# Optimization experiments

Measured on AMD Instinct MI355X. Metric: run time of the kernel, lower is better.

The kernel has to match this reference:

```python
import jax, jax.numpy as jnp
import numpy as np

TOPK = 9
N_CLASSES = 80
EPS = 1e-9


def bbox_iou(a, b):
    # a [N,4], b [M,4] xyxy -> [N,M]
    lt = jnp.maximum(a[:, None, :2], b[None, :, :2])
    rb = jnp.minimum(a[:, None, 2:], b[None, :, 2:])
    wh = jnp.clip(rb - lt, 0.0)
    inter = wh[..., 0] * wh[..., 1]
    area_a = (a[:, 2] - a[:, 0]) * (a[:, 3] - a[:, 1])
    area_b = (b[:, 2] - b[:, 0]) * (b[:, 3] - b[:, 1])
    return inter / (area_a[:, None] + area_b[None, :] - inter + EPS)


def atss_forward(anchor_bboxes, n_level_bboxes, gt_labels, gt_bboxes, mask_gt, pred_bboxes):
    na = anchor_bboxes.shape[0]
    bs, nmax = gt_bboxes.shape[:2]
    dt = gt_bboxes.dtype
    gt_flat = gt_bboxes.reshape(-1, 4)                       # [bs*nmax, 4]
    overlaps = bbox_iou(gt_flat, anchor_bboxes).reshape(bs, nmax, na)
    gt_c = (gt_flat[:, :2] + gt_flat[:, 2:]) * 0.5           # [bs*nmax, 2]
    an_c = (anchor_bboxes[:, :2] + anchor_bboxes[:, 2:]) * 0.5  # [na, 2]
    distances = jnp.sqrt(((gt_c[:, None, :] - an_c[None, :, :]) ** 2).sum(-1)).reshape(bs, nmax, na)

    # per-level topk candidate selection (levels are static python ints)
    mask_gt_b = mask_gt > 0                                  # [bs, nmax, 1]
    rows = jnp.arange(bs * nmax)[:, None]
    is_in_topk_list, topk_idx_list = [], []
    start = 0
    for nL in n_level_bboxes:
        k = min(TOPK, nL)
        d = distances[..., start:start + nL]
        _, idxs = jax.lax.top_k(-d, k)                       # closest-k -> [bs,nmax,k]
        topk_idx_list.append(idxs + start)
        idx_m = jnp.where(mask_gt_b, idxs, 0).reshape(bs * nmax, k)
        counts = jnp.zeros((bs * nmax, nL), dt).at[rows, idx_m].add(1.0)
        counts = counts.reshape(bs, nmax, nL)
        is_in_topk_list.append(jnp.where(counts > 1, jnp.zeros((), dt), counts))
        start += nL
    is_in_topk = jnp.concatenate(is_in_topk_list, -1)        # [bs,nmax,na]
    topk_idxs = jnp.concatenate(topk_idx_list, -1)           # [bs,nmax,sum_k]

    # adaptive threshold = mean + std of candidate IoUs (unbiased std, as torch)
    cand_ov = jnp.where(is_in_topk > 0, overlaps, 0.0)
    gathered = jnp.take_along_axis(cand_ov.reshape(bs * nmax, na),
                                   topk_idxs.reshape(bs * nmax, -1), axis=1)
    gathered = gathered.reshape(bs, nmax, -1)
    thr = gathered.mean(-1, keepdims=True) + jnp.std(gathered, axis=-1, ddof=1, keepdims=True)
    is_pos = jnp.where(cand_ov > thr, is_in_topk, 0.0)

    # anchor center strictly inside GT box
    lt = an_c[None, :, :] - gt_flat[:, None, :2]
    rb = gt_flat[:, None, 2:] - an_c[None, :, :]
    in_gt = (jnp.concatenate([lt, rb], -1).min(-1) > EPS).astype(dt).reshape(bs, nmax, na)

    mask_pos = is_pos * in_gt * mask_gt                      # mask_gt broadcasts [bs,nmax,1]

    # collision fix: anchors assigned to multiple GTs keep highest-IoU GT
    mps = mask_pos.sum(-2)                                   # [bs, na]
    multi = (mps[:, None, :] > 1)                            # [bs,1,na] broadcast
    is_max = jax.nn.one_hot(overlaps.argmax(1), nmax, dtype=dt).transpose(0, 2, 1)
    mask_pos = jnp.where(multi, is_max, mask_pos)
    mps = mask_pos.sum(-2)
    assigned_gt_idx = mask_pos.argmax(-2)                    # [bs, na]

    # final gathers
    flat_idx = assigned_gt_idx + jnp.arange(bs)[:, None] * nmax
    labels = gt_labels.reshape(-1)[flat_idx]                 # [bs, na]
    boxes = gt_bboxes.reshape(-1, 4)[flat_idx]               # [bs, na, 4]
    labels = jnp.where(mps > 0, labels, N_CLASSES)
    scores = jax.nn.one_hot(labels, N_CLASSES + 1, dtype=dt)[..., :N_CLASSES]

    # rescale scores by IoU(gt, pred) on positive anchors
    pious = jax.vmap(bbox_iou)(gt_bboxes, pred_bboxes) * mask_pos  # [bs,nmax,na]
    scores = scores * pious.max(-2)[..., None]
    return labels, boxes, scores, (mps > 0)


def setup_inputs():
    key = jax.random.key(0)
    ks = jax.random.split(key, 4)
    bs, nmax, img = 32, 100, 640
    strides = [8, 16, 32]
    anchors, nlb = [], []
    for s in strides:
        n = img // s
        xy = (np.stack(np.meshgrid(np.arange(n), np.arange(n), indexing='ij'), -1)
              .reshape(-1, 2).astype(np.float32) + 0.5) * s
        half = 2.5 * s
        anchors.append(np.concatenate([xy - half, xy + half], -1))
        nlb.append(n * n)
    anchor_bboxes = jnp.asarray(np.concatenate(anchors, 0), jnp.float32)  # [8400,4]
    na = anchor_bboxes.shape[0]

    def rand_boxes(k, shape):
        k1, k2 = jax.random.split(k)
        xy = jax.random.uniform(k1, shape + (2,), jnp.float32) * 520.0
        wh = jax.random.uniform(k2, shape + (2,), jnp.float32) * 112.0 + 8.0
        return jnp.concatenate([xy, xy + wh], -1)

    gt_bboxes = rand_boxes(ks[0], (bs, nmax))
    pred_bboxes = rand_boxes(ks[1], (bs, na))
    gt_labels = jax.random.randint(ks[2], (bs, nmax, 1), 0, N_CLASSES)
    mask_gt = (jax.random.uniform(ks[3], (bs, nmax, 1)) < 0.8).astype(jnp.float32)
    return {"anchor_bboxes": anchor_bboxes, "n_level_bboxes": nlb,
            "gt_labels": gt_labels, "gt_bboxes": gt_bboxes,
            "mask_gt": mask_gt, "pred_bboxes": pred_bboxes}


def reference(anchor_bboxes, n_level_bboxes, gt_labels, gt_bboxes, mask_gt, pred_bboxes):
    return atss_forward(anchor_bboxes, n_level_bboxes, gt_labels, gt_bboxes, mask_gt, pred_bboxes)
```

## Files before the change

### kernel.cpp

```cpp
#include <hip/hip_runtime.h>
#include <cstdint>
#include <cstddef>

#define BS   32
#define NMAX 100
#define NA   8400
#define NTOP 9
#define NLEV 3
#define NCLS 80

#define LAB_OFF 0
#define BOX_OFF (BS * NA)
#define SC_OFF  (BS * NA * 5)
#define FG_OFF  (BS * NA * 5 + BS * NA * NCLS)

__device__ __forceinline__ float iou_ab(float ax1, float ay1, float ax2, float ay2,
                                        float bx1, float by1, float bx2, float by2) {
    float ltx = fmaxf(ax1, bx1), lty = fmaxf(ay1, by1);
    float rbx = fminf(ax2, bx2), rby = fminf(ay2, by2);
    float w = fmaxf(__fsub_rn(rbx, ltx), 0.0f);
    float h = fmaxf(__fsub_rn(rby, lty), 0.0f);
    float inter = __fmul_rn(w, h);
    float aa = __fmul_rn(__fsub_rn(ax2, ax1), __fsub_rn(ay2, ay1));
    float ab = __fmul_rn(__fsub_rn(bx2, bx1), __fsub_rn(by2, by1));
    float den = __fadd_rn(__fadd_rn(__fadd_rn(aa, ab), -inter), 1e-9f);
    return __fdiv_rn(inter, den);
}

__global__ __launch_bounds__(256) void zero_ws(uint4* __restrict__ p, int n4) {
    const int i = blockIdx.x * 256 + threadIdx.x;
    if (i < n4) p[i] = make_uint4(0u, 0u, 0u, 0u);
}

__global__ __launch_bounds__(256) void atss_phase1(
    const float* __restrict__ anchors,
    const float* __restrict__ gt_bboxes,
    const float* __restrict__ mask_gt,
    unsigned* __restrict__ packed)
{
    const int wid  = (blockIdx.x << 2) + (threadIdx.x >> 6);
    const int lane = threadIdx.x & 63;
    if (wid >= BS * NMAX) return;
    if (mask_gt[wid] <= 0.0f) return;
    const int b = wid / NMAX;
    const int g = wid - b * NMAX;

    const float4 gtb = reinterpret_cast<const float4*>(gt_bboxes)[wid];
    const float gx1 = gtb.x, gy1 = gtb.y, gx2 = gtb.z, gy2 = gtb.w;
    const float gcx = __fmul_rn(__fadd_rn(gx1, gx2), 0.5f);
    const float gcy = __fmul_rn(__fadd_rn(gy1, gy2), 0.5f);

    const int   lev_start[NLEV] = {0, 6400, 8000};
    const int   lev_n[NLEV]     = {80, 40, 20};
    const float lev_s[NLEV]     = {8.f, 16.f, 32.f};

    int my_sel = 0;

    for (int L = 0; L < NLEV; ++L) {
        const int   n     = lev_n[L];
        const float s     = lev_s[L];
        const int   start = lev_start[L];

        const int ixn = (int)floorf(gcx / s - 0.5f + 0.5f);
        const int iyn = (int)floorf(gcy / s - 0.5f + 0.5f);
        const int wx = min(max(ixn - 3, 0), n - 7);
        const int wy = min(max(iyn - 3, 0), n - 7);

        unsigned long long key = ~0ull;
        int aidx = 0;
        if (lane < 49) {
            const int cix = wx + lane / 7;
            const int ciy = wy + lane % 7;
            aidx = start + cix * n + ciy;
            const float4 ab = reinterpret_cast<const float4*>(anchors)[aidx];
            const float acx = __fmul_rn(__fadd_rn(ab.x, ab.z), 0.5f);
            const float acy = __fmul_rn(__fadd_rn(ab.y, ab.w), 0.5f);
            const float dx = __fsub_rn(gcx, acx);
            const float dy = __fsub_rn(gcy, acy);
            const float d = sqrtf(__fadd_rn(__fmul_rn(dx, dx), __fmul_rn(dy, dy)));
            key = ((unsigned long long)__float_as_uint(d) << 32) | (unsigned)aidx;
        }

        int rank = 0;
#pragma unroll
        for (int j = 0; j < 49; ++j) {
            const unsigned long long kj = (unsigned long long)__shfl((long long)key, j);
            rank += (kj < key) ? 1 : 0;
        }

        const int dst = (rank < NTOP) ? (L * NTOP + rank) : 63;
        const int got = __builtin_amdgcn_ds_permute(dst << 2, aidx);
        if (lane >= L * NTOP && lane < L * NTOP + NTOP) my_sel = got;
    }

    float ov = 0.0f, acx = 0.0f, acy = 0.0f;
    if (lane < NLEV * NTOP) {
        const float4 ab = reinterpret_cast<const float4*>(anchors)[my_sel];
        ov  = iou_ab(gx1, gy1, gx2, gy2, ab.x, ab.y, ab.z, ab.w);
        acx = __fmul_rn(__fadd_rn(ab.x, ab.z), 0.5f);
        acy = __fmul_rn(__fadd_rn(ab.y, ab.w), 0.5f);
    }

    float sum = 0.0f;
#pragma unroll
    for (int j = 0; j < NLEV * NTOP; ++j) sum = __fadd_rn(sum, __shfl(ov, j));
    const float mean = __fdiv_rn(sum, 27.0f);
    float v = 0.0f;
#pragma unroll
    for (int j = 0; j < NLEV * NTOP; ++j) {
        const float dlt = __fsub_rn(__shfl(ov, j), mean);
        v = __fadd_rn(v, __fmul_rn(dlt, dlt));
    }
    const float thr = __fadd_rn(mean, sqrtf(__fdiv_rn(v, 26.0f)));

    if (lane < NLEV * NTOP && ov > thr) {
        const float m2 = fminf(fminf(__fsub_rn(acx, gx1), __fsub_rn(acy, gy1)),
                               fminf(__fsub_rn(gx2, acx), __fsub_rn(gy2, acy)));
        if (m2 > 1e-9f) {
            atomicAdd(&packed[b * NA + my_sel], (1u << 16) | (unsigned)g);
        }
    }
}

__global__ __launch_bounds__(256) void atss_phase2(
    const float* __restrict__ anchors,
    const float* __restrict__ gt_bboxes,
    const int*   __restrict__ gt_labels,
    const float* __restrict__ pred_bboxes,
    const unsigned* __restrict__ packed,
    float* __restrict__ out)
{
    const int b = blockIdx.y;
    const int tid = threadIdx.x;
    const int a0 = blockIdx.x * 256;
    const int a = a0 + tid;

    __shared__ float4 s_gt[NMAX];
    __shared__ int    s_lab[NMAX];
    __shared__ int    s_olab[256];
    __shared__ float  s_piou[256];

    for (int i = tid; i < NMAX; i += 256) {
        s_gt[i]  = reinterpret_cast<const float4*>(gt_bboxes)[b * NMAX + i];
        s_lab[i] = gt_labels[b * NMAX + i];
    }
    __syncthreads();

    int   label = NCLS;
    float piou  = 0.0f;

    if (a < NA) {
        const unsigned pk = packed[b * NA + a];
        const int c = (int)(pk >> 16);
        int  gstar    = 0;
        bool assigned = false;
        if (c == 1) {
            gstar = (int)(pk & 0xffffu);
            assigned = true;
        } else if (c > 1) {
            const float4 ab = reinterpret_cast<const float4*>(anchors)[a];
            float best = -INFINITY;
            int   bg = 0;
            for (int gg = 0; gg < NMAX; ++gg) {
                const float4 gb = s_gt[gg];
                float iou = iou_ab(gb.x, gb.y, gb.z, gb.w, ab.x, ab.y, ab.z, ab.w);
                if (iou > best) { best = iou; bg = gg; }
            }
            gstar = bg;
            assigned = true;
        }

        const float4 gb = s_gt[gstar];
        out[LAB_OFF + b * NA + a] = assigned ? (float)s_lab[gstar] : (float)NCLS;
        reinterpret_cast<float4*>(out + BOX_OFF)[b * NA + a] = gb;
        out[FG_OFF + b * NA + a] = assigned ? 1.0f : 0.0f;

        if (assigned) {
            label = s_lab[gstar];
            const float4 pb = reinterpret_cast<const float4*>(pred_bboxes)[b * NA + a];
            piou = iou_ab(gb.x, gb.y, gb.z, gb.w, pb.x, pb.y, pb.z, pb.w);
        }
    }

    s_olab[tid] = label;
    s_piou[tid] = piou;
    __syncthreads();

    const int nA   = min(256, NA - a0);
    const int tot4 = nA * (NCLS / 4);
    float4* srow4 = reinterpret_cast<float4*>(out + SC_OFF + (size_t)(b * NA + a0) * NCLS);
    for (int e = tid; e < tot4; e += 256) {
        const int al = e / (NCLS / 4);
        const int c0 = (e - al * (NCLS / 4)) * 4;
        const int lb = s_olab[al];
        const float p = s_piou[al];
        float4 v;
        v.x = (lb == c0    ) ? p : 0.0f;
        v.y = (lb == c0 + 1) ? p : 0.0f;
        v.z = (lb == c0 + 2) ? p : 0.0f;
        v.w = (lb == c0 + 3) ? p : 0.0f;
        srow4[e] = v;
    }
}

extern "C" void kernel_launch(void* const* d_in, const int* in_sizes, int n_in,
                              void* d_out, int out_size, void* d_ws, size_t ws_size,
                              hipStream_t stream) {
    const float* anchors   = (const float*)d_in[0];
    const int*   gt_labels = (const int*)d_in[2];
    const float* gt_bboxes = (const float*)d_in[3];
    const float* mask_gt   = (const float*)d_in[4];
    const float* pred      = (const float*)d_in[5];
    float* out = (float*)d_out;

    unsigned* packed = (unsigned*)d_ws;

    const int n4 = (BS * NA) / 4;
    zero_ws<<<(n4 + 255) / 256, 256, 0, stream>>>((uint4*)d_ws, n4);

    atss_phase1<<<(BS * NMAX + 3) / 4, 256, 0, stream>>>(anchors, gt_bboxes, mask_gt, packed);

    dim3 grid2((NA + 255) / 256, BS);
    atss_phase2<<<grid2, 256, 0, stream>>>(anchors, gt_bboxes, gt_labels, pred, packed, out);
}
```

Baseline: 50.48 us.

## Fuse zero, phase1 and phase2 into one cooperative kernel with grid syncs

Replaces the three-kernel sequence with a single cooperative persistent kernel of 512 blocks. It zeroes the workspace, runs the per-GT candidate selection, and writes the per-anchor outputs, separated by grid-wide barriers. This removes two kernel launch gaps. In exchange it pays for grid.sync and loses parallelism, since phase2 now runs 1056 tiles over 512 blocks in a grid-stride loop. If the cooperative launch fails, it falls back to the original three launches.

Result: slower. 150.4 us (+197.9%).

```diff
diff --git a/kernel.cpp b/kernel.cpp
--- a/kernel.cpp
+++ b/kernel.cpp
@@ -1,6 +1,9 @@
 #include <hip/hip_runtime.h>
+#include <hip/hip_cooperative_groups.h>
 #include <cstdint>
 #include <cstddef>
+
+namespace cg = cooperative_groups;
 
 #define BS   32
 #define NMAX 100
@@ -8,6 +11,8 @@
 #define NTOP 9
 #define NLEV 3
 #define NCLS 80
+#define NTILE 33
+#define GRID_BLKS 512
 
 #define LAB_OFF 0
 #define BOX_OFF (BS * NA)
@@ -27,21 +32,12 @@
     return __fdiv_rn(inter, den);
 }
 
-__global__ __launch_bounds__(256) void zero_ws(uint4* __restrict__ p, int n4) {
-    const int i = blockIdx.x * 256 + threadIdx.x;
-    if (i < n4) p[i] = make_uint4(0u, 0u, 0u, 0u);
-}
-
-__global__ __launch_bounds__(256) void atss_phase1(
+__device__ __forceinline__ void phase1_wave(
+    int wid, int lane,
     const float* __restrict__ anchors,
     const float* __restrict__ gt_bboxes,
-    const float* __restrict__ mask_gt,
     unsigned* __restrict__ packed)
 {
-    const int wid  = (blockIdx.x << 2) + (threadIdx.x >> 6);
-    const int lane = threadIdx.x & 63;
-    if (wid >= BS * NMAX) return;
-    if (mask_gt[wid] <= 0.0f) return;
     const int b = wid / NMAX;
     const int g = wid - b * NMAX;
 
@@ -120,6 +116,129 @@
             atomicAdd(&packed[b * NA + my_sel], (1u << 16) | (unsigned)g);
         }
     }
+}
+
+__global__ __launch_bounds__(256, 2) void atss_fused(
+    const float* __restrict__ anchors,
+    const int*   __restrict__ gt_labels,
+    const float* __restrict__ gt_bboxes,
+    const float* __restrict__ mask_gt,
+    const float* __restrict__ pred_bboxes,
+    unsigned* __restrict__ packed,
+    float* __restrict__ out)
+{
+    cg::grid_group grid = cg::this_grid();
+    const int tid  = threadIdx.x;
+    const int gtid = blockIdx.x * 256 + tid;
+    const int nthr = GRID_BLKS * 256;
+
+    __shared__ float4 s_gt[NMAX];
+    __shared__ int    s_lab[NMAX];
+    __shared__ int    s_olab[256];
+    __shared__ float  s_piou[256];
+
+    uint4* p4 = reinterpret_cast<uint4*>(packed);
+    for (int i = gtid; i < (BS * NA) / 4; i += nthr)
+        p4[i] = make_uint4(0u, 0u, 0u, 0u);
+
+    grid.sync();
+
+    const int lane   = tid & 63;
+    const int wave0  = (blockIdx.x << 2) + (tid >> 6);
+    const int nwaves = GRID_BLKS * 4;
+    for (int wid = wave0; wid < BS * NMAX; wid += nwaves) {
+        if (mask_gt[wid] > 0.0f)
+            phase1_wave(wid, lane, anchors, gt_bboxes, packed);
+    }
+
+    grid.sync();
+
+    for (int tile = blockIdx.x; tile < BS * NTILE; tile += GRID_BLKS) {
+        const int b  = tile / NTILE;
+        const int a0 = (tile - b * NTILE) * 256;
+        const int a  = a0 + tid;
+
+        __syncthreads();
+        for (int i = tid; i < NMAX; i += 256) {
+            s_gt[i]  = reinterpret_cast<const float4*>(gt_bboxes)[b * NMAX + i];
+            s_lab[i] = gt_labels[b * NMAX + i];
+        }
+        __syncthreads();
+
+        int   label = NCLS;
+        float piou  = 0.0f;
+
+        if (a < NA) {
+            const unsigned pk = packed[b * NA + a];
+            const int c = (int)(pk >> 16);
+            int  gstar    = 0;
+            bool assigned = false;
+            if (c == 1) {
+                gstar = (int)(pk & 0xffffu);
+                assigned = true;
+            } else if (c > 1) {
+                const float4 ab = reinterpret_cast<const float4*>(anchors)[a];
+                float best = -INFINITY;
+                int   bg = 0;
+                for (int gg = 0; gg < NMAX; ++gg) {
+                    const float4 gb = s_gt[gg];
+                    float iou = iou_ab(gb.x, gb.y, gb.z, gb.w, ab.x, ab.y, ab.z, ab.w);
+                    if (iou > best) { best = iou; bg = gg; }
+                }
+                gstar = bg;
+                assigned = true;
+            }
+
+            const float4 gb = s_gt[gstar];
+            out[LAB_OFF + b * NA + a] = assigned ? (float)s_lab[gstar] : (float)NCLS;
+            reinterpret_cast<float4*>(out + BOX_OFF)[b * NA + a] = gb;
+            out[FG_OFF + b * NA + a] = assigned ? 1.0f : 0.0f;
+
+            if (assigned) {
+                label = s_lab[gstar];
+                const float4 pb = reinterpret_cast<const float4*>(pred_bboxes)[b * NA + a];
+                piou = iou_ab(gb.x, gb.y, gb.z, gb.w, pb.x, pb.y, pb.z, pb.w);
+            }
+        }
+
+        s_olab[tid] = label;
+        s_piou[tid] = piou;
+        __syncthreads();
+
+        const int nA   = min(256, NA - a0);
+        const int tot4 = nA * (NCLS / 4);
+        float4* srow4 = reinterpret_cast<float4*>(out + SC_OFF + (size_t)(b * NA + a0) * NCLS);
+        for (int e = tid; e < tot4; e += 256) {
+            const int al = e / (NCLS / 4);
+            const int c0 = (e - al * (NCLS / 4)) * 4;
+            const int lb = s_olab[al];
+            const float p = s_piou[al];
+            float4 vv;
+            vv.x = (lb == c0    ) ? p : 0.0f;
+            vv.y = (lb == c0 + 1) ? p : 0.0f;
+            vv.z = (lb == c0 + 2) ? p : 0.0f;
+            vv.w = (lb == c0 + 3) ? p : 0.0f;
+            srow4[e] = vv;
+        }
+    }
+}
+
+__global__ __launch_bounds__(256) void zero_ws(uint4* __restrict__ p, int n4) {
+    const int i = blockIdx.x * 256 + threadIdx.x;
+    if (i < n4) p[i] = make_uint4(0u, 0u, 0u, 0u);
+}
+
+__global__ __launch_bounds__(256) void atss_phase1(
+    const float* __restrict__ anchors,
+    const float* __restrict__ gt_bboxes,
+    const float* __restrict__ mask_gt,
+    unsigned* __restrict__ packed)
+{
+    const int wid  = (blockIdx.x << 2) + (threadIdx.x >> 6);
+    const int lane = threadIdx.x & 63;
+    if (wid >= BS * NMAX) return;
+    if (mask_gt[wid] <= 0.0f) return;
+    phase1_wave(wid, lane, anchors, gt_bboxes, packed);
 }
 
 __global__ __launch_bounds__(256) void atss_phase2(
@@ -194,12 +313,12 @@
         const int c0 = (e - al * (NCLS / 4)) * 4;
         const int lb = s_olab[al];
         const float p = s_piou[al];
-        float4 v;
-        v.x = (lb == c0    ) ? p : 0.0f;
-        v.y = (lb == c0 + 1) ? p : 0.0f;
-        v.z = (lb == c0 + 2) ? p : 0.0f;
-        v.w = (lb == c0 + 3) ? p : 0.0f;
-        srow4[e] = v;
+        float4 vv;
+        vv.x = (lb == c0    ) ? p : 0.0f;
+        vv.y = (lb == c0 + 1) ? p : 0.0f;
+        vv.z = (lb == c0 + 2) ? p : 0.0f;
+        vv.w = (lb == c0 + 3) ? p : 0.0f;
+        srow4[e] = vv;
     }
 }
 
@@ -212,14 +331,18 @@
     const float* mask_gt   = (const float*)d_in[4];
     const float* pred      = (const float*)d_in[5];
     float* out = (float*)d_out;
-
     unsigned* packed = (unsigned*)d_ws;
 
-    const int n4 = (BS * NA) / 4;
-    zero_ws<<<(n4 + 255) / 256, 256, 0, stream>>>((uint4*)d_ws, n4);
-
-    atss_phase1<<<(BS * NMAX + 3) / 4, 256, 0, stream>>>(anchors, gt_bboxes, mask_gt, packed);
-
-    dim3 grid2((NA + 255) / 256, BS);
-    atss_phase2<<<grid2, 256, 0, stream>>>(anchors, gt_bboxes, gt_labels, pred, packed, out);
-}
+    void* args[] = {(void*)&anchors, (void*)&gt_labels, (void*)&gt_bboxes,
+                    (void*)&mask_gt, (void*)&pred, (void*)&packed, (void*)&out};
+    hipError_t e = hipLaunchCooperativeKernel((const void*)atss_fused,
+                                              dim3(GRID_BLKS), dim3(256),
+                                              args, 0, stream);
+    if (e != hipSuccess) {
+        const int n4 = (BS * NA) / 4;
+        zero_ws<<<(n4 + 255) / 256, 256, 0, stream>>>((uint4*)d_ws, n4);
+        atss_phase1<<<(BS * NMAX + 3) / 4, 256, 0, stream>>>(anchors, gt_bboxes, mask_gt, packed);
+        dim3 grid2((NA + 255) / 256, BS);
+        atss_phase2<<<grid2, 256, 0, stream>>>(anchors, gt_bboxes, gt_labels, pred, packed, out);
+    }
+}
```

## Replace per-anchor atomic workspace with per-GT positive lists scanned in phase2

Applied to the files above, without the earlier changes.

Phase1 now records each GT's positive candidates as a 27-bit ballot mask plus its list of selected anchor indices, instead of atomically incrementing a per-anchor packed counter. Phase2 rebuilds per-anchor counts and the assigned GT in shared memory by scanning all of its batch's GT lists and keeping the entries that fall in its tile. This drops the zero-fill kernel launch and the global atomics. In exchange, every phase2 block scans 2700 entries and does shared-memory atomics.

Result: no change. 49.70 us (-1.6%).

```diff
diff --git a/kernel.cpp b/kernel.cpp
--- a/kernel.cpp
+++ b/kernel.cpp
@@ -8,11 +8,14 @@
 #define NTOP 9
 #define NLEV 3
 #define NCLS 80
+#define NSEL (NLEV * NTOP)
+#define SLOT_STRIDE 32
 
 #define LAB_OFF 0
 #define BOX_OFF (BS * NA)
 #define SC_OFF  (BS * NA * 5)
 #define FG_OFF  (BS * NA * 5 + BS * NA * NCLS)
+
 
 __device__ __forceinline__ float iou_ab(float ax1, float ay1, float ax2, float ay2,
                                         float bx1, float by1, float bx2, float by2) {
@@ -27,23 +30,22 @@
     return __fdiv_rn(inter, den);
 }
 
-__global__ __launch_bounds__(256) void zero_ws(uint4* __restrict__ p, int n4) {
-    const int i = blockIdx.x * 256 + threadIdx.x;
-    if (i < n4) p[i] = make_uint4(0u, 0u, 0u, 0u);
-}
-
 __global__ __launch_bounds__(256) void atss_phase1(
     const float* __restrict__ anchors,
     const float* __restrict__ gt_bboxes,
     const float* __restrict__ mask_gt,
-    unsigned* __restrict__ packed)
+    unsigned* __restrict__ masks,
+    int* __restrict__ pos_anchors)
 {
     const int wid  = (blockIdx.x << 2) + (threadIdx.x >> 6);
     const int lane = threadIdx.x & 63;
     if (wid >= BS * NMAX) return;
-    if (mask_gt[wid] <= 0.0f) return;
-    const int b = wid / NMAX;
-    const int g = wid - b * NMAX;
+
+    if (mask_gt[wid] <= 0.0f) {
+        if (lane == 0) masks[wid] = 0u;
+        return;
+    }
+    const int g = wid % NMAX;
 
     const float4 gtb = reinterpret_cast<const float4*>(gt_bboxes)[wid];
     const float gx1 = gtb.x, gy1 = gtb.y, gx2 = gtb.z, gy2 = gtb.w;
@@ -94,7 +96,7 @@
     }
 
     float ov = 0.0f, acx = 0.0f, acy = 0.0f;
-    if (lane < NLEV * NTOP) {
+    if (lane < NSEL) {
         const float4 ab = reinterpret_cast<const float4*>(anchors)[my_sel];
         ov  = iou_ab(gx1, gy1, gx2, gy2, ab.x, ab.y, ab.z, ab.w);
         acx = __fmul_rn(__fadd_rn(ab.x, ab.z), 0.5f);
@@ -103,23 +105,23 @@
 
     float sum = 0.0f;
 #pragma unroll
-    for (int j = 0; j < NLEV * NTOP; ++j) sum = __fadd_rn(sum, __shfl(ov, j));
+    for (int j = 0; j < NSEL; ++j) sum = __fadd_rn(sum, __shfl(ov, j));
     const float mean = __fdiv_rn(sum, 27.0f);
     float v = 0.0f;
 #pragma unroll
-    for (int j = 0; j < NLEV * NTOP; ++j) {
+    for (int j = 0; j < NSEL; ++j) {
         const float dlt = __fsub_rn(__shfl(ov, j), mean);
         v = __fadd_rn(v, __fmul_rn(dlt, dlt));
     }
     const float thr = __fadd_rn(mean, sqrtf(__fdiv_rn(v, 26.0f)));
 
-    if (lane < NLEV * NTOP && ov > thr) {
-        const float m2 = fminf(fminf(__fsub_rn(acx, gx1), __fsub_rn(acy, gy1)),
-                               fminf(__fsub_rn(gx2, acx), __fsub_rn(gy2, acy)));
-        if (m2 > 1e-9f) {
-            atomicAdd(&packed[b * NA + my_sel], (1u << 16) | (unsigned)g);
-        }
-    }
+    const float m2 = fminf(fminf(__fsub_rn(acx, gx1), __fsub_rn(acy, gy1)),
+                           fminf(__fsub_rn(gx2, acx), __fsub_rn(gy2, acy)));
+    const bool positive = (lane < NSEL) && (ov > thr) && (m2 > 1e-9f);
+    const unsigned long long bal = __ballot(positive);
+
+    if (lane == 0) masks[wid] = (unsigned)bal;
+    if (lane < NSEL) pos_anchors[wid * SLOT_STRIDE + lane] = my_sel;
 }
 
 __global__ __launch_bounds__(256) void atss_phase2(
@@ -127,7 +129,8 @@
     const float* __restrict__ gt_bboxes,
     const int*   __restrict__ gt_labels,
     const float* __restrict__ pred_bboxes,
-    const unsigned* __restrict__ packed,
+    const unsigned* __restrict__ masks,
+    const int* __restrict__ pos_anchors,
     float* __restrict__ out)
 {
     const int b = blockIdx.y;
@@ -135,14 +138,34 @@
     const int a0 = blockIdx.x * 256;
     const int a = a0 + tid;
 
-    __shared__ float4 s_gt[NMAX];
-    __shared__ int    s_lab[NMAX];
-    __shared__ int    s_olab[256];
-    __shared__ float  s_piou[256];
-
-    for (int i = tid; i < NMAX; i += 256) {
-        s_gt[i]  = reinterpret_cast<const float4*>(gt_bboxes)[b * NMAX + i];
-        s_lab[i] = gt_labels[b * NMAX + i];
+    __shared__ float4   s_gt[NMAX];
+    __shared__ int      s_lab[NMAX];
+    __shared__ unsigned s_mask[NMAX];
+    __shared__ int      s_cnt[256];
+    __shared__ int      s_gsum[256];
+    __shared__ int      s_olab[256];
+    __shared__ float    s_piou[256];
+
+    if (tid < NMAX) {
+        s_gt[tid]   = reinterpret_cast<const float4*>(gt_bboxes)[b * NMAX + tid];
+        s_lab[tid]  = gt_labels[b * NMAX + tid];
+        s_mask[tid] = masks[b * NMAX + tid];
+    }
+    s_cnt[tid]  = 0;
+    s_gsum[tid] = 0;
+    __syncthreads();
+
+    for (int e = tid; e < NMAX * NSEL; e += 256) {
+        const int g    = e / NSEL;
+        const int slot = e - g * NSEL;
+        if ((s_mask[g] >> slot) & 1u) {
+            const int aa  = pos_anchors[(b * NMAX + g) * SLOT_STRIDE + slot];
+            const int rel = aa - a0;
+            if (rel >= 0 && rel < 256) {
+                atomicAdd(&s_cnt[rel], 1);
+                atomicAdd(&s_gsum[rel], g);
+            }
+        }
     }
     __syncthreads();
 
@@ -150,12 +173,11 @@
     float piou  = 0.0f;
 
     if (a < NA) {
-        const unsigned pk = packed[b * NA + a];
-        const int c = (int)(pk >> 16);
+        const int c = s_cnt[tid];
         int  gstar    = 0;
         bool assigned = false;
         if (c == 1) {
-            gstar = (int)(pk & 0xffffu);
+            gstar = s_gsum[tid];
             assigned = true;
         } else if (c > 1) {
             const float4 ab = reinterpret_cast<const float4*>(anchors)[a];
@@ -194,12 +216,12 @@
         const int c0 = (e - al * (NCLS / 4)) * 4;
         const int lb = s_olab[al];
         const float p = s_piou[al];
-        float4 v;
-        v.x = (lb == c0    ) ? p : 0.0f;
-        v.y = (lb == c0 + 1) ? p : 0.0f;
-        v.z = (lb == c0 + 2) ? p : 0.0f;
-        v.w = (lb == c0 + 3) ? p : 0.0f;
-        srow4[e] = v;
+        float4 vv;
+        vv.x = (lb == c0    ) ? p : 0.0f;
+        vv.y = (lb == c0 + 1) ? p : 0.0f;
+        vv.z = (lb == c0 + 2) ? p : 0.0f;
+        vv.w = (lb == c0 + 3) ? p : 0.0f;
+        srow4[e] = vv;
     }
 }
 
@@ -213,13 +235,13 @@
     const float* pred      = (const float*)d_in[5];
     float* out = (float*)d_out;
 
-    unsigned* packed = (unsigned*)d_ws;
-
-    const int n4 = (BS * NA) / 4;
-    zero_ws<<<(n4 + 255) / 256, 256, 0, stream>>>((uint4*)d_ws, n4);
-
-    atss_phase1<<<(BS * NMAX + 3) / 4, 256, 0, stream>>>(anchors, gt_bboxes, mask_gt, packed);
+    unsigned* masks       = (unsigned*)d_ws;
+    int*      pos_anchors = (int*)d_ws + BS * NMAX;
+
+    atss_phase1<<<(BS * NMAX + 3) / 4, 256, 0, stream>>>(
+        anchors, gt_bboxes, mask_gt, masks, pos_anchors);
 
     dim3 grid2((NA + 255) / 256, BS);
-    atss_phase2<<<grid2, 256, 0, stream>>>(anchors, gt_bboxes, gt_labels, pred, packed, out);
-}
+    atss_phase2<<<grid2, 256, 0, stream>>>(
+        anchors, gt_bboxes, gt_labels, pred, masks, pos_anchors, out);
+}
```
